# Optimization experiments

Hardware: AMD Instinct MI355X
Metric: run time of the kernel (lower is better)

## Reference

```python
import jax, jax.numpy as jnp
import numpy as np

I, H, B, T = 4, 32, 1024, 512


def _gru_dir(x, w_ih, w_hh, b_ih, b_hh, reverse):
    # x: [B,T,in], w_ih: [3H,in], w_hh: [3H,H]. PyTorch gate order: r, z, n.
    xg = jnp.einsum('bti,gi->btg', x, w_ih) + b_ih  # [B,T,3H] precomputed input gates
    if reverse:
        xg = xg[:, ::-1]
    h0 = jnp.zeros((x.shape[0], w_hh.shape[1]), x.dtype)

    def step(h, xg_t):
        hg = h @ w_hh.T + b_hh
        xr, xz, xn = jnp.split(xg_t, 3, axis=-1)
        hr, hz, hn = jnp.split(hg, 3, axis=-1)
        r = jax.nn.sigmoid(xr + hr)
        z = jax.nn.sigmoid(xz + hz)
        n = jnp.tanh(xn + r * hn)
        h_new = (1.0 - z) * n + z * h
        return h_new, h_new

    _, ys = jax.lax.scan(step, h0, jnp.swapaxes(xg, 0, 1))  # [T,B,H]
    ys = jnp.swapaxes(ys, 0, 1)
    if reverse:
        ys = ys[:, ::-1]
    return ys


def _bigru(x, w_ih, w_hh, b_ih, b_hh):
    # stacked direction axis 0: [2,3H,in], etc.
    f = _gru_dir(x, w_ih[0], w_hh[0], b_ih[0], b_hh[0], reverse=False)
    b = _gru_dir(x, w_ih[1], w_hh[1], b_ih[1], b_hh[1], reverse=True)
    return jnp.concatenate([f, b], axis=-1)  # [B,T,2H]


def setup_inputs() -> dict:
    key = jax.random.key(0)
    ks = jax.random.split(key, 13)
    s = 0.1
    return {
        'x': jax.random.normal(ks[0], (B, T, I), dtype=jnp.float32),
        'w_ih_l0': jax.random.normal(ks[1], (2, 3 * H, I), dtype=jnp.float32) * s,
        'w_hh_l0': jax.random.normal(ks[2], (2, 3 * H, H), dtype=jnp.float32) * s,
        'b_ih_l0': jax.random.normal(ks[3], (2, 3 * H), dtype=jnp.float32) * s,
        'b_hh_l0': jax.random.normal(ks[4], (2, 3 * H), dtype=jnp.float32) * s,
        'w_ih_l1': jax.random.normal(ks[5], (2, 3 * H, 2 * H), dtype=jnp.float32) * s,
        'w_hh_l1': jax.random.normal(ks[6], (2, 3 * H, H), dtype=jnp.float32) * s,
        'b_ih_l1': jax.random.normal(ks[7], (2, 3 * H), dtype=jnp.float32) * s,
        'b_hh_l1': jax.random.normal(ks[8], (2, 3 * H), dtype=jnp.float32) * s,
        'attn_w': jax.random.normal(ks[9], (1, 2 * H), dtype=jnp.float32) * s,
        'attn_b': jax.random.normal(ks[10], (1,), dtype=jnp.float32) * s,
        'fc_w': jax.random.normal(ks[11], (1, 2 * H), dtype=jnp.float32) * s,
        'fc_b': jax.random.normal(ks[12], (1,), dtype=jnp.float32) * s,
    }


def reference(x, w_ih_l0, w_hh_l0, b_ih_l0, b_hh_l0, w_ih_l1, w_hh_l1, b_ih_l1, b_hh_l1, attn_w, attn_b, fc_w, fc_b):
    h1 = _bigru(x, w_ih_l0, w_hh_l0, b_ih_l0, b_hh_l0)   # [B,T,2H]
    out = _bigru(h1, w_ih_l1, w_hh_l1, b_ih_l1, b_hh_l1)  # [B,T,2H] (dropout inactive in eval)
    logits = out @ attn_w.T + attn_b                      # [B,T,1]
    attn = jax.nn.softmax(logits, axis=1)                 # softmax over time
    ctx = jnp.sum(attn * out, axis=1)                     # [B,2H]
    return jax.nn.sigmoid(ctx @ fc_w.T + fc_b)            # [B,1]
```

## Files before the change

### kernel.cpp

```cpp
#include <hip/hip_runtime.h>
#include <math.h>

#define BB 1024
#define TT 512
#define L2E 1.4426950408889634f

typedef __attribute__((ext_vector_type(4))) short  bfx4;
typedef __attribute__((ext_vector_type(8))) short  bfx8;
typedef __attribute__((ext_vector_type(2))) int    int2v;
typedef __attribute__((ext_vector_type(4))) int    int4v;
typedef __attribute__((ext_vector_type(4))) float  floatx4;

__device__ __forceinline__ float fast_rcp(float x){ return __builtin_amdgcn_rcpf(x); }
__device__ __forceinline__ float exp2f_(float x){ return __builtin_amdgcn_exp2f(x); }
__device__ __forceinline__ float sigmoidf_(float x){ return fast_rcp(1.0f + __expf(-x)); }
__device__ __forceinline__ unsigned short f2bf(float f){
    unsigned u = __builtin_bit_cast(unsigned, f);
    u += 0x7fffu + ((u >> 16) & 1u);
    return (unsigned short)(u >> 16);
}
__device__ __forceinline__ float bf2f(unsigned short u){
    return __builtin_bit_cast(float, ((unsigned)u) << 16);
}
__device__ __forceinline__ int cvt_pk_bf16(float lo, float hi){
    int r; asm("v_cvt_pk_bf16_f32 %0, %1, %2" : "=v"(r) : "v"(lo), "v"(hi)); return r;
}
__device__ __forceinline__ floatx4 mfma16(bfx4 a, bfx4 b, floatx4 c){
    return __builtin_amdgcn_mfma_f32_16x16x16bf16_1k(a, b, c, 0, 0, 0);
}
__device__ __forceinline__ floatx4 mfma32(bfx8 a, bfx8 b, floatx4 c){
    return __builtin_amdgcn_mfma_f32_16x16x32_bf16(a, b, c, 0, 0, 0);
}

__device__ __forceinline__ int sigma_k(int q, int j){
    return (j < 4) ? (q*4 + j) : (16 + q*4 + (j - 4));
}

__device__ __forceinline__ void lgkm_barrier(){
    __builtin_amdgcn_sched_barrier(0);
    asm volatile("s_waitcnt lgkmcnt(0)" ::: "memory");
    __builtin_amdgcn_s_barrier();
    __builtin_amdgcn_sched_barrier(0);
}

__global__ __launch_bounds__(128, 1) void gru_l0(
    const float* __restrict__ x,
    const float* __restrict__ w_ih,
    const float* __restrict__ w_hh,
    const float* __restrict__ b_ih,
    const float* __restrict__ b_hh,
    unsigned short* __restrict__ h1)
{
    const int tile = blockIdx.x;
    const int bt   = tile >> 1;
    const int d    = tile & 1;
    const int b0   = bt * 16;
    const int w    = threadIdx.x >> 6;
    const int L    = threadIdx.x & 63;
    const int c    = L & 15;
    const int q    = L >> 4;

    bfx8 whh[3];
    bfx4 wih[3];
    #pragma unroll
    for (int g = 0; g < 3; ++g){
        const float sc = (g == 2) ? (2.0f * L2E) : L2E;
        const int row = d*96 + g*32 + w*16 + c;
        bfx8 f;
        #pragma unroll
        for (int j = 0; j < 8; ++j)
            f[j] = f2bf(w_hh[(size_t)row*32 + sigma_k(q, j)] * sc);
        whh[g] = f;
        bfx4 fi = {0,0,0,0};
        if (q == 0){
            #pragma unroll
            for (int j = 0; j < 4; ++j) fi[j] = f2bf(w_ih[(size_t)row*4 + j] * sc);
        }
        wih[g] = fi;
    }
    floatx4 cbr, cbz, cbni, cbhn;
    #pragma unroll
    for (int r = 0; r < 4; ++r){
        const int gidx = d*96 + w*16 + q*4 + r;
        cbr[r]  = L2E * (b_ih[gidx]      + b_hh[gidx]);
        cbz[r]  = L2E * (b_ih[gidx + 32] + b_hh[gidx + 32]);
        cbni[r] = 2.0f * L2E * b_ih[gidx + 64];
        cbhn[r] = 2.0f * L2E * b_hh[gidx + 64];
    }

    __shared__ int2v hx[2][2][64];

    float hr[4] = {0.f,0.f,0.f,0.f};
    bfx8 ahc = {0,0,0,0,0,0,0,0};

    const size_t xrow = (size_t)(b0 + c) * TT;
    float4 xq[4] = {{0,0,0,0},{0,0,0,0},{0,0,0,0},{0,0,0,0}};
    if (q == 0){
        #pragma unroll
        for (int p = 0; p < 4; ++p)
            xq[p] = *(const float4*)(x + (xrow + (d ? TT-1-p : p))*4);
    }

    for (int tb = 0; tb < TT; tb += 4){
        #pragma unroll
        for (int p = 0; p < 4; ++p){
            const int t = tb + p;
            bfx4 ax = {0,0,0,0};
            if (q == 0){
                int2v a; a[0] = cvt_pk_bf16(xq[p].x, xq[p].y); a[1] = cvt_pk_bf16(xq[p].z, xq[p].w);
                ax = __builtin_bit_cast(bfx4, a);
            }
            if (q == 0 && t + 4 < TT)
                xq[p] = *(const float4*)(x + (xrow + (d ? TT-5-t : t+4))*4);

            floatx4 racc  = mfma16(wih[0], ax, cbr);
            floatx4 zacc  = mfma16(wih[1], ax, cbz);
            floatx4 xnacc = mfma16(wih[2], ax, cbni);
            racc          = mfma32(whh[0], ahc, racc);
            zacc          = mfma32(whh[1], ahc, zacc);
            floatx4 hnacc = mfma32(whh[2], ahc, cbhn);

            #pragma unroll
            for (int r = 0; r < 4; ++r){
                const float pp = 1.0f + exp2f_(-racc[r]);
                const float qd = 1.0f + exp2f_(-zacc[r]);
                const float s  = fast_rcp(pp * qd);
                const float rg = s * qd;
                const float zg = s * pp;
                const float e2 = exp2f_(xnacc[r] + rg * hnacc[r]);
                const float ng = 1.0f - 2.0f * fast_rcp(e2 + 1.0f);
                hr[r] = ng + zg * (hr[r] - ng);
            }
            int2v own;
            own[0] = cvt_pk_bf16(hr[0], hr[1]);
            own[1] = cvt_pk_bf16(hr[2], hr[3]);

            const int tx = d ? (TT-1-t) : t;
            *(int2v*)(&h1[((size_t)(b0 + c)*TT + tx)*64 + d*32 + w*16 + q*4]) = own;

            const int wb = t & 1;
            hx[wb][w][L] = own;
            lgkm_barrier();
            const int2v oth = hx[wb][1 - w][L];

            int4v comb;
            if (w == 0){ comb[0] = own[0]; comb[1] = own[1]; comb[2] = oth[0]; comb[3] = oth[1]; }
            else       { comb[0] = oth[0]; comb[1] = oth[1]; comb[2] = own[0]; comb[3] = own[1]; }
            ahc = __builtin_bit_cast(bfx8, comb);
        }
    }
}

__global__ __launch_bounds__(128, 1) void gru_l1(
    const unsigned short* __restrict__ h1,
    const float* __restrict__ w_ih,
    const float* __restrict__ w_hh,
    const float* __restrict__ b_ih,
    const float* __restrict__ b_hh,
    unsigned short* __restrict__ out2)
{
    const int tile = blockIdx.x;
    const int bt   = tile >> 1;
    const int d    = tile & 1;
    const int b0   = bt * 16;
    const int w    = threadIdx.x >> 6;
    const int L    = threadIdx.x & 63;
    const int c    = L & 15;
    const int q    = L >> 4;

    bfx8 whh[3], wi0[3], wi1[3];
    #pragma unroll
    for (int g = 0; g < 3; ++g){
        const float sc = (g == 2) ? (2.0f * L2E) : L2E;
        const int row = d*96 + g*32 + w*16 + c;
        bfx8 f, g0, g1;
        #pragma unroll
        for (int j = 0; j < 8; ++j){
            f[j]  = f2bf(w_hh[(size_t)row*32 + sigma_k(q, j)] * sc);
            g0[j] = f2bf(w_ih[(size_t)row*64 +      q*8 + j] * sc);
            g1[j] = f2bf(w_ih[(size_t)row*64 + 32 + q*8 + j] * sc);
        }
        whh[g] = f; wi0[g] = g0; wi1[g] = g1;
    }
    floatx4 cbr, cbz, cbni, cbhn;
    #pragma unroll
    for (int r = 0; r < 4; ++r){
        const int gidx = d*96 + w*16 + q*4 + r;
        cbr[r]  = L2E * (b_ih[gidx]      + b_hh[gidx]);
        cbz[r]  = L2E * (b_ih[gidx + 32] + b_hh[gidx + 32]);
        cbni[r] = 2.0f * L2E * b_ih[gidx + 64];
        cbhn[r] = 2.0f * L2E * b_hh[gidx + 64];
    }

    __shared__ int2v hx[2][2][64];

    float hr[4] = {0.f,0.f,0.f,0.f};
    bfx8 ahc = {0,0,0,0,0,0,0,0};

    const size_t arow = (size_t)(b0 + c) * TT;
    bfx8 A0[4], A1[4];
    #pragma unroll
    for (int p = 0; p < 4; ++p){
        const int tx = d ? TT-1-p : p;
        A0[p] = *(const bfx8*)(&h1[(arow + tx)*64 +      q*8]);
        A1[p] = *(const bfx8*)(&h1[(arow + tx)*64 + 32 + q*8]);
    }

    for (int tb = 0; tb < TT; tb += 4){
        #pragma unroll
        for (int p = 0; p < 4; ++p){
            const int t = tb + p;

            floatx4 racc  = mfma32(wi0[0], A0[p], cbr);
            racc          = mfma32(wi1[0], A1[p], racc);
            floatx4 zacc  = mfma32(wi0[1], A0[p], cbz);
            zacc          = mfma32(wi1[1], A1[p], zacc);
            floatx4 xnacc = mfma32(wi0[2], A0[p], cbni);
            xnacc         = mfma32(wi1[2], A1[p], xnacc);

            if (t + 4 < TT){
                const int tx4 = d ? (TT-5-t) : (t+4);
                A0[p] = *(const bfx8*)(&h1[(arow + tx4)*64 +      q*8]);
                A1[p] = *(const bfx8*)(&h1[(arow + tx4)*64 + 32 + q*8]);
            }

            racc          = mfma32(whh[0], ahc, racc);
            zacc          = mfma32(whh[1], ahc, zacc);
            floatx4 hnacc = mfma32(whh[2], ahc, cbhn);

            #pragma unroll
            for (int r = 0; r < 4; ++r){
                const float pp = 1.0f + exp2f_(-racc[r]);
                const float qd = 1.0f + exp2f_(-zacc[r]);
                const float s  = fast_rcp(pp * qd);
                const float rg = s * qd;
                const float zg = s * pp;
                const float e2 = exp2f_(xnacc[r] + rg * hnacc[r]);
                const float ng = 1.0f - 2.0f * fast_rcp(e2 + 1.0f);
                hr[r] = ng + zg * (hr[r] - ng);
            }
            int2v own;
            own[0] = cvt_pk_bf16(hr[0], hr[1]);
            own[1] = cvt_pk_bf16(hr[2], hr[3]);

            const int tx = d ? (TT-1-t) : t;
            *(int2v*)(&out2[((size_t)(b0 + c)*TT + tx)*64 + d*32 + w*16 + q*4]) = own;

            const int wb = t & 1;
            hx[wb][w][L] = own;
            lgkm_barrier();
            const int2v oth = hx[wb][1 - w][L];

            int4v comb;
            if (w == 0){ comb[0] = own[0]; comb[1] = own[1]; comb[2] = oth[0]; comb[3] = oth[1]; }
            else       { comb[0] = oth[0]; comb[1] = oth[1]; comb[2] = own[0]; comb[3] = own[1]; }
            ahc = __builtin_bit_cast(bfx8, comb);
        }
    }
}

__global__ __launch_bounds__(256) void attn_fc(
    const unsigned short* __restrict__ out2,
    const float* __restrict__ attn_w, const float* __restrict__ attn_b,
    const float* __restrict__ fc_w,   const float* __restrict__ fc_b,
    float* __restrict__ out)
{
    const int b    = blockIdx.x;
    const int tid  = threadIdx.x;
    const int wave = tid >> 6;
    const int lane = tid & 63;
    const int sub  = lane >> 3;
    const int cg   = lane & 7;
    const int st   = wave*8 + sub;

    __shared__ float m_sh[32], s_sh[32];
    __shared__ float acc_sh[32][64];

    float aw[8];
    #pragma unroll
    for (int j = 0; j < 8; ++j) aw[j] = attn_w[cg*8 + j];
    const float ab = attn_b[0];

    float m = -INFINITY, s = 0.0f;
    float acc[8] = {0,0,0,0,0,0,0,0};

    for (int t = st; t < TT; t += 32){
        const bfx8 v8 = *(const bfx8*)(&out2[((size_t)b*TT + t)*64 + cg*8]);
        float v[8];
        #pragma unroll
        for (int j = 0; j < 8; ++j) v[j] = bf2f((unsigned short)v8[j]);
        float p = v[0]*aw[0];
        #pragma unroll
        for (int j = 1; j < 8; ++j) p += v[j]*aw[j];
        p += __shfl_xor(p, 1, 64);
        p += __shfl_xor(p, 2, 64);
        p += __shfl_xor(p, 4, 64);
        const float logit = p + ab;
        const float nm = fmaxf(m, logit);
        const float cs = exp2f_((m - nm) * L2E);
        const float ce = exp2f_((logit - nm) * L2E);
        s = s * cs + ce;
        #pragma unroll
        for (int j = 0; j < 8; ++j) acc[j] = acc[j]*cs + ce*v[j];
        m = nm;
    }
    if (cg == 0){ m_sh[st] = m; s_sh[st] = s; }
    #pragma unroll
    for (int j = 0; j < 8; ++j) acc_sh[st][cg*8 + j] = acc[j];
    __syncthreads();

    if (wave == 0){
        float M = m_sh[0];
        #pragma unroll
        for (int w = 1; w < 32; ++w) M = fmaxf(M, m_sh[w]);
        float S = 0.0f, ctx = 0.0f;
        #pragma unroll 4
        for (int w = 0; w < 32; ++w){
            const float cw = exp2f_((m_sh[w] - M) * L2E);
            S   += s_sh[w] * cw;
            ctx += acc_sh[w][lane] * cw;
        }
        float v = ctx * fast_rcp(S) * fc_w[lane];
        #pragma unroll
        for (int off = 32; off > 0; off >>= 1) v += __shfl_xor(v, off, 64);
        if (lane == 0) out[b] = sigmoidf_(v + fc_b[0]);
    }
}

extern "C" void kernel_launch(void* const* d_in, const int* in_sizes, int n_in,
                              void* d_out, int out_size, void* d_ws, size_t ws_size,
                              hipStream_t stream) {
    (void)in_sizes; (void)n_in; (void)out_size; (void)ws_size;
    const float* x      = (const float*)d_in[0];
    const float* w_ih0  = (const float*)d_in[1];
    const float* w_hh0  = (const float*)d_in[2];
    const float* b_ih0  = (const float*)d_in[3];
    const float* b_hh0  = (const float*)d_in[4];
    const float* w_ih1  = (const float*)d_in[5];
    const float* w_hh1  = (const float*)d_in[6];
    const float* b_ih1  = (const float*)d_in[7];
    const float* b_hh1  = (const float*)d_in[8];
    const float* attn_w = (const float*)d_in[9];
    const float* attn_b = (const float*)d_in[10];
    const float* fc_w   = (const float*)d_in[11];
    const float* fc_b   = (const float*)d_in[12];
    float* out = (float*)d_out;

    unsigned short* h1 = (unsigned short*)d_ws;
    unsigned short* o2 = (unsigned short*)((char*)d_ws + 134217728);

    gru_l0<<<128, 128, 0, stream>>>(x, w_ih0, w_hh0, b_ih0, b_hh0, h1);
    gru_l1<<<128, 128, 0, stream>>>(h1, w_ih1, w_hh1, b_ih1, b_hh1, o2);
    attn_fc<<<BB, 256, 0, stream>>>(o2, attn_w, attn_b, fc_w, fc_b, out);
}
```

Baseline: 409.8 us.

## Split GRU gate elementwise work across duplicated waves and prefetch attention loads

```diff
diff --git a/kernel.cpp b/kernel.cpp
--- a/kernel.cpp
+++ b/kernel.cpp
@@ -43,7 +43,19 @@
     __builtin_amdgcn_sched_barrier(0);
 }
 
-__global__ __launch_bounds__(128, 1) void gru_l0(
+#define GATE_ELEM(r, hidx)                                                     \
+    {                                                                          \
+        const float pp = 1.0f + exp2f_(-racc[r]);                              \
+        const float qd = 1.0f + exp2f_(-zacc[r]);                              \
+        const float s  = fast_rcp(pp * qd);                                    \
+        const float rg = s * qd;                                               \
+        const float zg = s * pp;                                               \
+        const float e2 = exp2f_(xnacc[r] + rg * hnacc[r]);                     \
+        const float ng = 1.0f - 2.0f * fast_rcp(e2 + 1.0f);                    \
+        hr[hidx] = ng + zg * (hr[hidx] - ng);                                  \
+    }
+
+__global__ __launch_bounds__(256, 1) void gru_l0(
     const float* __restrict__ x,
     const float* __restrict__ w_ih,
     const float* __restrict__ w_hh,
@@ -55,7 +67,9 @@
     const int bt   = tile >> 1;
     const int d    = tile & 1;
     const int b0   = bt * 16;
-    const int w    = threadIdx.x >> 6;
+    const int wv   = threadIdx.x >> 6;
+    const int w    = wv >> 1;
+    const int e    = wv & 1;
     const int L    = threadIdx.x & 63;
     const int c    = L & 15;
     const int q    = L >> 4;
@@ -88,9 +102,9 @@
         cbhn[r] = 2.0f * L2E * b_hh[gidx + 64];
     }
 
-    __shared__ int2v hx[2][2][64];
-
-    float hr[4] = {0.f,0.f,0.f,0.f};
+    __shared__ int hx[2][4][64];
+
+    float hr[2] = {0.f, 0.f};
     bfx8 ahc = {0,0,0,0,0,0,0,0};
 
     const size_t xrow = (size_t)(b0 + c) * TT;
@@ -120,38 +134,27 @@
             zacc          = mfma32(whh[1], ahc, zacc);
             floatx4 hnacc = mfma32(whh[2], ahc, cbhn);
 
-            #pragma unroll
-            for (int r = 0; r < 4; ++r){
-                const float pp = 1.0f + exp2f_(-racc[r]);
-                const float qd = 1.0f + exp2f_(-zacc[r]);
-                const float s  = fast_rcp(pp * qd);
-                const float rg = s * qd;
-                const float zg = s * pp;
-                const float e2 = exp2f_(xnacc[r] + rg * hnacc[r]);
-                const float ng = 1.0f - 2.0f * fast_rcp(e2 + 1.0f);
-                hr[r] = ng + zg * (hr[r] - ng);
-            }
-            int2v own;
-            own[0] = cvt_pk_bf16(hr[0], hr[1]);
-            own[1] = cvt_pk_bf16(hr[2], hr[3]);
+            if (e == 0){ GATE_ELEM(0, 0); GATE_ELEM(1, 1); }
+            else       { GATE_ELEM(2, 0); GATE_ELEM(3, 1); }
+            const int own = cvt_pk_bf16(hr[0], hr[1]);
 
             const int tx = d ? (TT-1-t) : t;
-            *(int2v*)(&h1[((size_t)(b0 + c)*TT + tx)*64 + d*32 + w*16 + q*4]) = own;
+            *(int*)(&h1[((size_t)(b0 + c)*TT + tx)*64 + d*32 + w*16 + q*4 + 2*e]) = own;
 
             const int wb = t & 1;
-            hx[wb][w][L] = own;
+            hx[wb][2*w + e][L] = own;
             lgkm_barrier();
-            const int2v oth = hx[wb][1 - w][L];
-
             int4v comb;
-            if (w == 0){ comb[0] = own[0]; comb[1] = own[1]; comb[2] = oth[0]; comb[3] = oth[1]; }
-            else       { comb[0] = oth[0]; comb[1] = oth[1]; comb[2] = own[0]; comb[3] = own[1]; }
+            comb[0] = hx[wb][0][L];
+            comb[1] = hx[wb][1][L];
+            comb[2] = hx[wb][2][L];
+            comb[3] = hx[wb][3][L];
             ahc = __builtin_bit_cast(bfx8, comb);
         }
     }
 }
 
-__global__ __launch_bounds__(128, 1) void gru_l1(
+__global__ __launch_bounds__(256, 1) void gru_l1(
     const unsigned short* __restrict__ h1,
     const float* __restrict__ w_ih,
     const float* __restrict__ w_hh,
@@ -163,7 +166,9 @@
     const int bt   = tile >> 1;
     const int d    = tile & 1;
     const int b0   = bt * 16;
-    const int w    = threadIdx.x >> 6;
+    const int wv   = threadIdx.x >> 6;
+    const int w    = wv >> 1;
+    const int e    = wv & 1;
     const int L    = threadIdx.x & 63;
     const int c    = L & 15;
     const int q    = L >> 4;
@@ -192,9 +197,9 @@
         cbhn[r] = 2.0f * L2E * b_hh[gidx + 64];
     }
 
-    __shared__ int2v hx[2][2][64];
-
-    float hr[4] = {0.f,0.f,0.f,0.f};
+    __shared__ int hx[2][4][64];
+
+    float hr[2] = {0.f, 0.f};
     bfx8 ahc = {0,0,0,0,0,0,0,0};
 
     const size_t arow = (size_t)(b0 + c) * TT;
@@ -228,32 +233,21 @@
             zacc          = mfma32(whh[1], ahc, zacc);
             floatx4 hnacc = mfma32(whh[2], ahc, cbhn);
 
-            #pragma unroll
-            for (int r = 0; r < 4; ++r){
-                const float pp = 1.0f + exp2f_(-racc[r]);
-                const float qd = 1.0f + exp2f_(-zacc[r]);
-                const float s  = fast_rcp(pp * qd);
-                const float rg = s * qd;
-                const float zg = s * pp;
-                const float e2 = exp2f_(xnacc[r] + rg * hnacc[r]);
-                const float ng = 1.0f - 2.0f * fast_rcp(e2 + 1.0f);
-                hr[r] = ng + zg * (hr[r] - ng);
-            }
-            int2v own;
-            own[0] = cvt_pk_bf16(hr[0], hr[1]);
-            own[1] = cvt_pk_bf16(hr[2], hr[3]);
+            if (e == 0){ GATE_ELEM(0, 0); GATE_ELEM(1, 1); }
+            else       { GATE_ELEM(2, 0); GATE_ELEM(3, 1); }
+            const int own = cvt_pk_bf16(hr[0], hr[1]);
 
             const int tx = d ? (TT-1-t) : t;
-            *(int2v*)(&out2[((size_t)(b0 + c)*TT + tx)*64 + d*32 + w*16 + q*4]) = own;
+            *(int*)(&out2[((size_t)(b0 + c)*TT + tx)*64 + d*32 + w*16 + q*4 + 2*e]) = own;
 
             const int wb = t & 1;
-            hx[wb][w][L] = own;
+            hx[wb][2*w + e][L] = own;
             lgkm_barrier();
-            const int2v oth = hx[wb][1 - w][L];
-
             int4v comb;
-            if (w == 0){ comb[0] = own[0]; comb[1] = own[1]; comb[2] = oth[0]; comb[3] = oth[1]; }
-            else       { comb[0] = oth[0]; comb[1] = oth[1]; comb[2] = own[0]; comb[3] = own[1]; }
+            comb[0] = hx[wb][0][L];
+            comb[1] = hx[wb][1][L];
+            comb[2] = hx[wb][2][L];
+            comb[3] = hx[wb][3][L];
             ahc = __builtin_bit_cast(bfx8, comb);
         }
     }
@@ -284,25 +278,35 @@
     float m = -INFINITY, s = 0.0f;
     float acc[8] = {0,0,0,0,0,0,0,0};
 
-    for (int t = st; t < TT; t += 32){
-        const bfx8 v8 = *(const bfx8*)(&out2[((size_t)b*TT + t)*64 + cg*8]);
-        float v[8];
-        #pragma unroll
-        for (int j = 0; j < 8; ++j) v[j] = bf2f((unsigned short)v8[j]);
-        float p = v[0]*aw[0];
-        #pragma unroll
-        for (int j = 1; j < 8; ++j) p += v[j]*aw[j];
-        p += __shfl_xor(p, 1, 64);
-        p += __shfl_xor(p, 2, 64);
-        p += __shfl_xor(p, 4, 64);
-        const float logit = p + ab;
-        const float nm = fmaxf(m, logit);
-        const float cs = exp2f_((m - nm) * L2E);
-        const float ce = exp2f_((logit - nm) * L2E);
-        s = s * cs + ce;
-        #pragma unroll
-        for (int j = 0; j < 8; ++j) acc[j] = acc[j]*cs + ce*v[j];
-        m = nm;
+    const unsigned short* base = &out2[(size_t)b*TT*64 + cg*8];
+    bfx8 vq[4];
+    #pragma unroll
+    for (int p = 0; p < 4; ++p) vq[p] = *(const bfx8*)(base + (size_t)(st + 32*p)*64);
+
+    for (int ib = 0; ib < 4; ++ib){
+        #pragma unroll
+        for (int p = 0; p < 4; ++p){
+            const int it = ib*4 + p;
+            const bfx8 v8 = vq[p];
+            if (it + 4 < 16) vq[p] = *(const bfx8*)(base + (size_t)(st + 32*(it+4))*64);
+            float v[8];
+            #pragma unroll
+            for (int j = 0; j < 8; ++j) v[j] = bf2f((unsigned short)v8[j]);
+            float p_ = v[0]*aw[0];
+            #pragma unroll
+            for (int j = 1; j < 8; ++j) p_ += v[j]*aw[j];
+            p_ += __shfl_xor(p_, 1, 64);
+            p_ += __shfl_xor(p_, 2, 64);
+            p_ += __shfl_xor(p_, 4, 64);
+            const float logit = p_ + ab;
+            const float nm = fmaxf(m, logit);
+            const float cs = exp2f_((m - nm) * L2E);
+            const float ce = exp2f_((logit - nm) * L2E);
+            s = s * cs + ce;
+            #pragma unroll
+            for (int j = 0; j < 8; ++j) acc[j] = acc[j]*cs + ce*v[j];
+            m = nm;
+        }
     }
     if (cg == 0){ m_sh[st] = m; s_sh[st] = s; }
     #pragma unroll
@@ -349,7 +353,7 @@
     unsigned short* h1 = (unsigned short*)d_ws;
     unsigned short* o2 = (unsigned short*)((char*)d_ws + 134217728);
 
-    gru_l0<<<128, 128, 0, stream>>>(x, w_ih0, w_hh0, b_ih0, b_hh0, h1);
-    gru_l1<<<128, 128, 0, stream>>>(h1, w_ih1, w_hh1, b_ih1, b_hh1, o2);
+    gru_l0<<<128, 256, 0, stream>>>(x, w_ih0, w_hh0, b_ih0, b_hh0, h1);
+    gru_l1<<<128, 256, 0, stream>>>(h1, w_ih1, w_hh1, b_ih1, b_hh1, o2);
     attn_fc<<<BB, 256, 0, stream>>>(o2, attn_w, attn_b, fc_w, fc_b, out);
 }
```

After: 412.2 us. No clear change (+0.6%).
